# Kernel tuning notes

Hardware: AMD Instinct MI355X
Metric: run time of the kernel (lower is better)

Reference implementation:

```python
import jax, jax.numpy as jnp
import numpy as np

B, T, C = 2, 2048, 1024
H = 16
HD = C // H  # 64
SCALE = 0.1 / (HD ** 0.5)


def setup_inputs() -> dict:
    key = jax.random.key(0)
    k1, k2, k3 = jax.random.split(key, 3)
    x = jax.random.normal(k1, (B, T, C), dtype=jnp.float32)
    W_attn = jax.random.normal(k2, (C, 3 * C), dtype=jnp.float32) * (C ** -0.5)
    b_attn = jnp.zeros((3 * C,), dtype=jnp.float32)
    W_proj = jax.random.normal(k3, (C, C), dtype=jnp.float32) * (C ** -0.5)
    b_proj = jnp.zeros((C,), dtype=jnp.float32)
    return {"x": x, "W_attn": W_attn, "b_attn": b_attn, "W_proj": W_proj, "b_proj": b_proj}


def reference(x, W_attn, b_attn, W_proj, b_proj):
    Bx, Tx, Cx = x.shape
    qkv = x @ W_attn + b_attn  # [B,T,3C]
    q, k, v = jnp.split(qkv, 3, axis=-1)
    # [B,T,C] -> [B,H,T,HD]
    q = q.reshape(Bx, Tx, H, HD).transpose(0, 2, 1, 3)
    k = k.reshape(Bx, Tx, H, HD).transpose(0, 2, 1, 3)
    v = v.reshape(Bx, Tx, H, HD).transpose(0, 2, 1, 3)
    # note the extra 0.1 factor baked into this module's scaling
    attn = jnp.einsum('bhqd,bhkd->bhqk', q, k) * SCALE
    causal = jnp.tril(jnp.ones((Tx, Tx), dtype=bool))
    attn = jnp.where(causal[None, None, :, :], attn, -jnp.inf)
    attn = jax.nn.softmax(attn, axis=-1)
    y = jnp.einsum('bhqk,bhkd->bhqd', attn, v)
    y = y.transpose(0, 2, 1, 3).reshape(Bx, Tx, Cx)
    return y @ W_proj + b_proj
```

## Files before the change

### kernel.cpp

```cpp
#include <hip/hip_runtime.h>

typedef unsigned short u16;
typedef unsigned int u32;
typedef float f32x4 __attribute__((ext_vector_type(4)));
typedef float f32x16 __attribute__((ext_vector_type(16)));
typedef __bf16 bf16x8 __attribute__((ext_vector_type(8)));
typedef u16 u16x8 __attribute__((ext_vector_type(8)));
typedef u32 u32x4 __attribute__((ext_vector_type(4)));

#define ATT_SCALE 0.0125f
#define LOG2E 1.4426950408889634f

__device__ __forceinline__ u16 f2bf(float x) {
  unsigned u = __builtin_bit_cast(unsigned, x);
  u += 0x7fffu + ((u >> 16) & 1u);
  return (u16)(u >> 16);
}

__device__ __forceinline__ u32 pack_bf16(float lo, float hi) {
  __bf16 a = (__bf16)lo, b = (__bf16)hi;
  return ((u32)__builtin_bit_cast(u16, b) << 16) | __builtin_bit_cast(u16, a);
}

__device__ __forceinline__ float fexp2(float x) {
  return __builtin_amdgcn_exp2f(x);
}

__device__ __forceinline__ f32x4 mfma16(u16x8 a, u16x8 b, f32x4 c) {
  return __builtin_amdgcn_mfma_f32_16x16x32_bf16(
      __builtin_bit_cast(bf16x8, a), __builtin_bit_cast(bf16x8, b), c, 0, 0, 0);
}

__device__ __forceinline__ f32x16 mfma32(u16x8 a, u16x8 b, f32x16 c) {
  return __builtin_amdgcn_mfma_f32_32x32x16_bf16(
      __builtin_bit_cast(bf16x8, a), __builtin_bit_cast(bf16x8, b), c, 0, 0, 0);
}

__device__ __forceinline__ void gl_lds16(const void* g, void* l) {
  __builtin_amdgcn_global_load_lds(
      (__attribute__((address_space(1))) void*)g,
      (__attribute__((address_space(3))) void*)l, 16, 0, 0);
}

__global__ void k_pre(const float* __restrict__ x, const float* __restrict__ W_attn,
                      const float* __restrict__ W_proj, u16* __restrict__ x_bf,
                      u16* __restrict__ Wt_a, u16* __restrict__ Wt_p) {
  __shared__ float tile[32][33];
  const int id = blockIdx.x, tid = threadIdx.x;
  if (id < 2048) {
    int base = id * 2048 + tid * 4;
#pragma unroll
    for (int s = 0; s < 2; ++s) {
      int i = base + s * 1024;
      float4 v = *(const float4*)&x[i];
      ushort4 o;
      o.x = f2bf(v.x); o.y = f2bf(v.y); o.z = f2bf(v.z); o.w = f2bf(v.w);
      *(ushort4*)&x_bf[i] = o;
    }
    return;
  }
  const float* in;
  u16* outp;
  int rows, cols, bx, by;
  if (id < 5120) {
    int t2 = id - 2048;
    bx = t2 % 96; by = t2 / 96;
    in = W_attn; outp = Wt_a; rows = 1024; cols = 3072;
  } else {
    int t3 = id - 5120;
    bx = t3 & 31; by = t3 >> 5;
    in = W_proj; outp = Wt_p; rows = 1024; cols = 1024;
  }
  int tx = tid & 31, ty = tid >> 5;
  int n0 = bx * 32, k0 = by * 32;
#pragma unroll
  for (int i = 0; i < 32; i += 8)
    tile[ty + i][tx] = in[(size_t)(k0 + ty + i) * cols + n0 + tx];
  __syncthreads();
#pragma unroll
  for (int i = 0; i < 32; i += 8)
    outp[(size_t)(n0 + ty + i) * rows + k0 + tx] = f2bf(tile[tx][ty + i]);
}

__global__ void k_gemm_qkv(const u16* __restrict__ A, const u16* __restrict__ Bt,
                           const float* __restrict__ bias,
                           u16* __restrict__ qb, u16* __restrict__ kb, u16* __restrict__ vTb) {
  __shared__ u16 Al[128 * 64];
  __shared__ u16 Bl[128 * 64];
  const int tid = threadIdx.x;
  const int lane = tid & 63;
  const int w = tid >> 6;
  const int m0 = blockIdx.y * 128;
  const int n0 = blockIdx.x * 128;
  const int wr = (w >> 1) * 64;
  const int wc = (w & 1) * 64;
  const int lr = lane & 15;
  const int lk = (lane >> 4) * 8;

  f32x4 acc[4][4] = {};

  for (int k0 = 0; k0 < 1024; k0 += 64) {
#pragma unroll
    for (int it = 0; it < 4; ++it) {
      int off = (it * 256 + tid) * 8;
      int r = off >> 6, c = off & 63;
      gl_lds16(&A[(size_t)(m0 + r) * 1024 + k0 + c], &Al[off]);
      gl_lds16(&Bt[(size_t)(n0 + r) * 1024 + k0 + c], &Bl[off]);
    }
    __syncthreads();
#pragma unroll
    for (int kk = 0; kk < 64; kk += 32) {
      u16x8 af[4], bf[4];
#pragma unroll
      for (int i = 0; i < 4; ++i) {
        af[i] = *(const u16x8*)&Al[(wr + i * 16 + lr) * 64 + kk + lk];
        bf[i] = *(const u16x8*)&Bl[(wc + i * 16 + lr) * 64 + kk + lk];
      }
#pragma unroll
      for (int i = 0; i < 4; ++i)
#pragma unroll
        for (int j = 0; j < 4; ++j)
          acc[i][j] = mfma16(af[i], bf[j], acc[i][j]);
    }
    __syncthreads();
  }

#pragma unroll
  for (int i = 0; i < 4; ++i) {
    int rowb = m0 + wr + i * 16 + ((lane >> 4) << 2);
#pragma unroll
    for (int j = 0; j < 4; ++j) {
      int col = n0 + wc + j * 16 + lr;
      float bv = bias[col];
      int which = col >> 10;
      int c = col & 1023;
      int h = c >> 6, d = c & 63;
      int b_ = rowb >> 11, t0 = rowb & 2047;
      int bh = b_ * 16 + h;
      if (which == 2) {
        ushort4 st;
        st.x = f2bf(acc[i][j][0] + bv);
        st.y = f2bf(acc[i][j][1] + bv);
        st.z = f2bf(acc[i][j][2] + bv);
        st.w = f2bf(acc[i][j][3] + bv);
        *(ushort4*)&vTb[((size_t)bh * 64 + d) * 2048 + t0] = st;
      } else {
        u16* dst = (which == 0) ? qb : kb;
        float sc = (which == 0) ? (ATT_SCALE * LOG2E) : 1.0f;
#pragma unroll
        for (int r = 0; r < 4; ++r) {
          float fv = (acc[i][j][r] + bv) * sc;
          dst[((size_t)bh * 2048 + t0 + r) * 64 + d] = f2bf(fv);
        }
      }
    }
  }
}

__device__ __forceinline__ void stage_pair(const u16* __restrict__ kb_bh,
                                           const u16* __restrict__ vT_bh,
                                           u16* Kd, u16* Vd, int kv0, int tid) {
#pragma unroll
  for (int it = 0; it < 4; ++it) {
    int ch = it * 256 + tid;
    int r = ch >> 3, c = ch & 7;
    gl_lds16(&kb_bh[(size_t)(kv0 + r) * 64 + (c ^ (r & 7)) * 8], &Kd[ch * 8]);
    int r2 = ch >> 4, c2 = ch & 15;
    int h2 = c2 >> 3, cc = c2 & 7;
    gl_lds16(&vT_bh[(size_t)r2 * 2048 + kv0 + (h2 * 8 + (cc ^ (r2 & 7))) * 8],
             &Vd[ch * 8]);
  }
}

__global__ __launch_bounds__(256) void k_attn(const u16* __restrict__ qb,
                                              const u16* __restrict__ kb,
                                              const u16* __restrict__ vTb,
                                              u16* __restrict__ yb) {
  __shared__ u16 Kl[2][8192];
  __shared__ u16 Vl[2][8192];

  const int tid = threadIdx.x, lane = tid & 63, w = tid >> 6;
  const int wq = w & 1;
  const int wp = w >> 1;
  const int id = blockIdx.x;
  const int bh = (id & 7) + ((id >> 7) << 3);
  const int pairi = (id >> 3) & 15;
  const int b_ = bh >> 4, h = bh & 15;
  const int ql = lane & 31;
  const int hi = lane >> 5;

  const u16* kb_bh = kb + (size_t)bh * 2048 * 64;
  const u16* vT_bh = vTb + (size_t)bh * 64 * 2048;

#pragma unroll 1
  for (int phase = 0; phase < 2; ++phase) {
    const int qt = phase ? (31 - pairi) : pairi;
    const int q0w = qt * 64 + wq * 32;
    const int qg = q0w + ql;
    const int lim = wq * 32 + ql;

    const u16* qrow = qb + ((size_t)bh * 2048 + qg) * 64;
    u16x8 qf[4];
#pragma unroll
    for (int ks = 0; ks < 4; ++ks)
      qf[ks] = *(const u16x8*)&qrow[ks * 16 + hi * 8];

    f32x16 o0 = {}, o1 = {};
    float mrow = -1e30f, lrow = 0.f;

    const int nkv = qt + 1;
    const int niter = (nkv + 1) >> 1;
    stage_pair(kb_bh, vT_bh, Kl[0], Vl[0], 0, tid);
    __syncthreads();
    int cur = 0;

    for (int it = 0; it < niter; ++it) {
      if (it + 1 < niter)
        stage_pair(kb_bh, vT_bh, Kl[cur ^ 1], Vl[cur ^ 1], (it + 1) * 128, tid);

      const int mytile = 2 * it + wp;
      if (mytile <= qt) {
        const u16* Kc = Kl[cur];
        const u16* Vc = Vl[cur];
        const int rbase = wp * 64;

        f32x16 s0 = {}, s1 = {};
        __builtin_amdgcn_s_setprio(1);
#pragma unroll
        for (int ks = 0; ks < 4; ++ks) {
          int ch = 2 * ks + hi;
          int r0 = rbase + ql, r1 = rbase + 32 + ql;
          u16x8 kf0 = *(const u16x8*)&Kc[r0 * 64 + ((ch ^ (r0 & 7)) * 8)];
          u16x8 kf1 = *(const u16x8*)&Kc[r1 * 64 + ((ch ^ (r1 & 7)) * 8)];
          s0 = mfma32(kf0, qf[ks], s0);
          s1 = mfma32(kf1, qf[ks], s1);
        }
        __builtin_amdgcn_s_setprio(0);

        const bool diag = (mytile == qt);
        float pv[32];
        float tmax = -1e30f;
#pragma unroll
        for (int r = 0; r < 16; ++r) {
          float a = s0[r], b2 = s1[r];
          if (diag) {
            int kl0 = (r & 3) + 8 * (r >> 2) + 4 * hi;
            if (kl0 > lim) a = -1e30f;
            if (kl0 + 32 > lim) b2 = -1e30f;
          }
          pv[r] = a;
          pv[16 + r] = b2;
          tmax = fmaxf(tmax, fmaxf(a, b2));
        }
        float rmax = fmaxf(tmax, __shfl_xor(tmax, 32, 64));

        if (__any(rmax > mrow + 8.0f)) {
          float mn = fmaxf(mrow, rmax);
          float al = fexp2(mrow - mn);
          mrow = mn;
          lrow *= al;
#pragma unroll
          for (int r = 0; r < 16; ++r) { o0[r] *= al; o1[r] *= al; }
        }

        u32 pw[16];
#pragma unroll
        for (int j = 0; j < 16; ++j) {
          float e0 = fexp2(pv[2 * j] - mrow);
          float e1 = fexp2(pv[2 * j + 1] - mrow);
          lrow += e0 + e1;
          pw[j] = pack_bf16(e0, e1);
        }

#pragma unroll
        for (int tt = 0; tt < 2; ++tt)
#pragma unroll
          for (int u = 0; u < 2; ++u)
#pragma unroll
            for (int z = 0; z < 2; ++z) {
              int jA = tt * 8 + u * 4 + z;
              asm volatile("v_permlane32_swap_b32 %0, %1"
                           : "+v"(pw[jA]), "+v"(pw[jA + 2]));
            }

        __builtin_amdgcn_s_setprio(1);
#pragma unroll
        for (int ks = 0; ks < 4; ++ks) {
          u32x4 pwv = {pw[4 * ks], pw[4 * ks + 1], pw[4 * ks + 2], pw[4 * ks + 3]};
          u16x8 pfrag = __builtin_bit_cast(u16x8, pwv);
          int ch = 2 * ks + hi;
          int rv0 = ql, rv1 = 32 + ql;
          u16x8 vf0 = *(const u16x8*)&Vc[rv0 * 128 + (wp * 8 + (ch ^ (rv0 & 7))) * 8];
          u16x8 vf1 = *(const u16x8*)&Vc[rv1 * 128 + (wp * 8 + (ch ^ (rv1 & 7))) * 8];
          o0 = mfma32(vf0, pfrag, o0);
          o1 = mfma32(vf1, pfrag, o1);
        }
        __builtin_amdgcn_s_setprio(0);
      }
      __syncthreads();
      cur ^= 1;
    }

    float* mb = (float*)&Kl[0][0];
    if (wp == 1) {
      float4* dst = (float4*)&mb[(wq * 64 + lane) * 37];
      float4 hd; hd.x = mrow; hd.y = lrow; hd.z = 0.f; hd.w = 0.f;
      dst[0] = hd;
#pragma unroll
      for (int j = 0; j < 4; ++j) {
        float4 t0 = {o0[4 * j], o0[4 * j + 1], o0[4 * j + 2], o0[4 * j + 3]};
        float4 t1 = {o1[4 * j], o1[4 * j + 1], o1[4 * j + 2], o1[4 * j + 3]};
        dst[1 + j] = t0;
        dst[5 + j] = t1;
      }
    }
    __syncthreads();
    if (wp == 0) {
      const float4* src = (const float4*)&mb[(wq * 64 + lane) * 37];
      float4 hd = src[0];
      float m2 = hd.x, l2 = hd.y;
      float m = fmaxf(mrow, m2);
      float a1 = fexp2(mrow - m), a2 = fexp2(m2 - m);
      float l = lrow * a1 + l2 * a2;
      l += __shfl_xor(l, 32, 64);
      float inv = 1.0f / l;

      size_t ybase = ((size_t)b_ * 2048 + qg) * 1024 + h * 64;
#pragma unroll
      for (int dt = 0; dt < 2; ++dt) {
#pragma unroll
        for (int rg = 0; rg < 4; ++rg) {
          float4 po = src[1 + dt * 4 + rg];
          const f32x16& ov = dt ? o1 : o0;
          int d0 = dt * 32 + 8 * rg + 4 * hi;
          ushort4 st;
          st.x = f2bf((ov[rg * 4 + 0] * a1 + po.x * a2) * inv);
          st.y = f2bf((ov[rg * 4 + 1] * a1 + po.y * a2) * inv);
          st.z = f2bf((ov[rg * 4 + 2] * a1 + po.z * a2) * inv);
          st.w = f2bf((ov[rg * 4 + 3] * a1 + po.w * a2) * inv);
          *(ushort4*)&yb[ybase + d0] = st;
        }
      }
    }
    __syncthreads();
  }
}

__global__ void k_gemm_out(const u16* __restrict__ A, const u16* __restrict__ Bt,
                           const float* __restrict__ bias, float* __restrict__ out) {
  __shared__ u16 Al[64 * 64];
  __shared__ u16 Bl[128 * 64];
  const int tid = threadIdx.x;
  const int lane = tid & 63;
  const int w = tid >> 6;
  const int m0 = blockIdx.y * 64;
  const int n0 = blockIdx.x * 128;
  const int wr = (w >> 1) * 32;
  const int wc = (w & 1) * 64;
  const int lr = lane & 15;
  const int lk = (lane >> 4) * 8;

  f32x4 acc[2][4] = {};

  for (int k0 = 0; k0 < 1024; k0 += 64) {
#pragma unroll
    for (int it = 0; it < 2; ++it) {
      int ch = it * 256 + tid;
      int r = ch >> 3, c = (ch & 7) * 8;
      gl_lds16(&A[(size_t)(m0 + r) * 1024 + k0 + c], &Al[ch * 8]);
    }
#pragma unroll
    for (int it = 0; it < 4; ++it) {
      int ch = it * 256 + tid;
      int r = ch >> 3, c = (ch & 7) * 8;
      gl_lds16(&Bt[(size_t)(n0 + r) * 1024 + k0 + c], &Bl[ch * 8]);
    }
    __syncthreads();
#pragma unroll
    for (int kk = 0; kk < 64; kk += 32) {
      u16x8 af[2], bf[4];
#pragma unroll
      for (int i = 0; i < 2; ++i)
        af[i] = *(const u16x8*)&Al[(wr + i * 16 + lr) * 64 + kk + lk];
#pragma unroll
      for (int j = 0; j < 4; ++j)
        bf[j] = *(const u16x8*)&Bl[(wc + j * 16 + lr) * 64 + kk + lk];
#pragma unroll
      for (int i = 0; i < 2; ++i)
#pragma unroll
        for (int j = 0; j < 4; ++j)
          acc[i][j] = mfma16(af[i], bf[j], acc[i][j]);
    }
    __syncthreads();
  }

#pragma unroll
  for (int i = 0; i < 2; ++i) {
    int rowb = m0 + wr + i * 16 + ((lane >> 4) << 2);
#pragma unroll
    for (int j = 0; j < 4; ++j) {
      int col = n0 + wc + j * 16 + lr;
      float bv = bias[col];
#pragma unroll
      for (int r = 0; r < 4; ++r)
        out[(size_t)(rowb + r) * 1024 + col] = acc[i][j][r] + bv;
    }
  }
}

extern "C" void kernel_launch(void* const* d_in, const int* in_sizes, int n_in,
                              void* d_out, int out_size, void* d_ws, size_t ws_size,
                              hipStream_t stream) {
  const float* x      = (const float*)d_in[0];
  const float* W_attn = (const float*)d_in[1];
  const float* b_attn = (const float*)d_in[2];
  const float* W_proj = (const float*)d_in[3];
  const float* b_proj = (const float*)d_in[4];
  float* out = (float*)d_out;

  char* ws = (char*)d_ws;
  const size_t MB = 1024 * 1024;
  u16* x_bf  = (u16*)(ws);
  u16* Wt_a  = (u16*)(ws + 8 * MB);
  u16* Wt_p  = (u16*)(ws + 14 * MB);
  u16* qbf   = (u16*)(ws + 16 * MB);
  u16* kbf   = (u16*)(ws + 24 * MB);
  u16* vTbf  = (u16*)(ws + 32 * MB);
  u16* ybf   = (u16*)(ws + 40 * MB);

  k_pre<<<6144, 256, 0, stream>>>(x, W_attn, W_proj, x_bf, Wt_a, Wt_p);
  k_gemm_qkv<<<dim3(24, 32), 256, 0, stream>>>(x_bf, Wt_a, b_attn, qbf, kbf, vTbf);
  k_attn<<<512, 256, 0, stream>>>(qbf, kbf, vTbf, ybf);
  k_gemm_out<<<dim3(8, 64), 256, 0, stream>>>(ybf, Wt_p, b_proj, out);
}
```

Measured before the change: 112.4 us.

## Split attention KV tile across 8 waves with 4-way partial softmax merge

Doubles the attention block to 512 threads so each 64-key KV tile is split into two 32-key halves handled by separate waves, giving four independent softmax partials per query group. A three-step online-softmax merge through LDS then combines them. Each wave does half the QK and PV MFMA work per tile, which cuts per-wave latency and register pressure. In exchange it adds more merge traffic, more exp/rescale work and a larger block that may lower occupancy.

```diff
diff --git a/kernel.cpp b/kernel.cpp
--- a/kernel.cpp
+++ b/kernel.cpp
@@ -161,8 +161,8 @@
                                            const u16* __restrict__ vT_bh,
                                            u16* Kd, u16* Vd, int kv0, int tid) {
 #pragma unroll
-  for (int it = 0; it < 4; ++it) {
-    int ch = it * 256 + tid;
+  for (int it = 0; it < 2; ++it) {
+    int ch = it * 512 + tid;
     int r = ch >> 3, c = ch & 7;
     gl_lds16(&kb_bh[(size_t)(kv0 + r) * 64 + (c ^ (r & 7)) * 8], &Kd[ch * 8]);
     int r2 = ch >> 4, c2 = ch & 15;
@@ -172,16 +172,17 @@
   }
 }
 
-__global__ __launch_bounds__(256) void k_attn(const u16* __restrict__ qb,
+__global__ __launch_bounds__(512) void k_attn(const u16* __restrict__ qb,
                                               const u16* __restrict__ kb,
                                               const u16* __restrict__ vTb,
                                               u16* __restrict__ yb) {
-  __shared__ u16 Kl[2][8192];
-  __shared__ u16 Vl[2][8192];
+  __shared__ u16 lds_[32768];
 
   const int tid = threadIdx.x, lane = tid & 63, w = tid >> 6;
   const int wq = w & 1;
-  const int wp = w >> 1;
+  const int pid = w >> 1;
+  const int wp = pid & 1;
+  const int wk = pid >> 1;
   const int id = blockIdx.x;
   const int bh = (id & 7) + ((id >> 7) << 3);
   const int pairi = (id >> 3) & 15;
@@ -210,47 +211,42 @@
 
     const int nkv = qt + 1;
     const int niter = (nkv + 1) >> 1;
-    stage_pair(kb_bh, vT_bh, Kl[0], Vl[0], 0, tid);
+    stage_pair(kb_bh, vT_bh, lds_, lds_ + 16384, 0, tid);
     __syncthreads();
     int cur = 0;
 
     for (int it = 0; it < niter; ++it) {
       if (it + 1 < niter)
-        stage_pair(kb_bh, vT_bh, Kl[cur ^ 1], Vl[cur ^ 1], (it + 1) * 128, tid);
+        stage_pair(kb_bh, vT_bh, lds_ + (cur ^ 1) * 8192,
+                   lds_ + 16384 + (cur ^ 1) * 8192, (it + 1) * 128, tid);
 
       const int mytile = 2 * it + wp;
       if (mytile <= qt) {
-        const u16* Kc = Kl[cur];
-        const u16* Vc = Vl[cur];
-        const int rbase = wp * 64;
-
-        f32x16 s0 = {}, s1 = {};
+        const u16* Kc = lds_ + cur * 8192;
+        const u16* Vc = lds_ + 16384 + cur * 8192;
+        const int rk = wp * 64 + wk * 32 + ql;
+
+        f32x16 s0 = {};
         __builtin_amdgcn_s_setprio(1);
 #pragma unroll
         for (int ks = 0; ks < 4; ++ks) {
           int ch = 2 * ks + hi;
-          int r0 = rbase + ql, r1 = rbase + 32 + ql;
-          u16x8 kf0 = *(const u16x8*)&Kc[r0 * 64 + ((ch ^ (r0 & 7)) * 8)];
-          u16x8 kf1 = *(const u16x8*)&Kc[r1 * 64 + ((ch ^ (r1 & 7)) * 8)];
-          s0 = mfma32(kf0, qf[ks], s0);
-          s1 = mfma32(kf1, qf[ks], s1);
+          u16x8 kf = *(const u16x8*)&Kc[rk * 64 + ((ch ^ (rk & 7)) * 8)];
+          s0 = mfma32(kf, qf[ks], s0);
         }
         __builtin_amdgcn_s_setprio(0);
 
         const bool diag = (mytile == qt);
-        float pv[32];
         float tmax = -1e30f;
 #pragma unroll
         for (int r = 0; r < 16; ++r) {
-          float a = s0[r], b2 = s1[r];
+          float a = s0[r];
           if (diag) {
-            int kl0 = (r & 3) + 8 * (r >> 2) + 4 * hi;
-            if (kl0 > lim) a = -1e30f;
-            if (kl0 + 32 > lim) b2 = -1e30f;
+            int kl = wk * 32 + (r & 3) + 8 * (r >> 2) + 4 * hi;
+            if (kl > lim) a = -1e30f;
+            s0[r] = a;
           }
-          pv[r] = a;
-          pv[16 + r] = b2;
-          tmax = fmaxf(tmax, fmaxf(a, b2));
+          tmax = fmaxf(tmax, a);
         }
         float rmax = fmaxf(tmax, __shfl_xor(tmax, 32, 64));
 
@@ -263,35 +259,31 @@
           for (int r = 0; r < 16; ++r) { o0[r] *= al; o1[r] *= al; }
         }
 
-        u32 pw[16];
-#pragma unroll
-        for (int j = 0; j < 16; ++j) {
-          float e0 = fexp2(pv[2 * j] - mrow);
-          float e1 = fexp2(pv[2 * j + 1] - mrow);
+        u32 pw[8];
+#pragma unroll
+        for (int j = 0; j < 8; ++j) {
+          float e0 = fexp2(s0[2 * j] - mrow);
+          float e1 = fexp2(s0[2 * j + 1] - mrow);
           lrow += e0 + e1;
           pw[j] = pack_bf16(e0, e1);
         }
 
 #pragma unroll
-        for (int tt = 0; tt < 2; ++tt)
-#pragma unroll
-          for (int u = 0; u < 2; ++u)
-#pragma unroll
-            for (int z = 0; z < 2; ++z) {
-              int jA = tt * 8 + u * 4 + z;
-              asm volatile("v_permlane32_swap_b32 %0, %1"
-                           : "+v"(pw[jA]), "+v"(pw[jA + 2]));
-            }
+        for (int g = 0; g < 2; ++g)
+#pragma unroll
+          for (int z = 0; z < 2; ++z)
+            asm volatile("v_permlane32_swap_b32 %0, %1"
+                         : "+v"(pw[g * 4 + z]), "+v"(pw[g * 4 + z + 2]));
 
         __builtin_amdgcn_s_setprio(1);
 #pragma unroll
-        for (int ks = 0; ks < 4; ++ks) {
+        for (int ks = 0; ks < 2; ++ks) {
           u32x4 pwv = {pw[4 * ks], pw[4 * ks + 1], pw[4 * ks + 2], pw[4 * ks + 3]};
           u16x8 pfrag = __builtin_bit_cast(u16x8, pwv);
-          int ch = 2 * ks + hi;
+          int cc = wk * 4 + 2 * ks + hi;
           int rv0 = ql, rv1 = 32 + ql;
-          u16x8 vf0 = *(const u16x8*)&Vc[rv0 * 128 + (wp * 8 + (ch ^ (rv0 & 7))) * 8];
-          u16x8 vf1 = *(const u16x8*)&Vc[rv1 * 128 + (wp * 8 + (ch ^ (rv1 & 7))) * 8];
+          u16x8 vf0 = *(const u16x8*)&Vc[rv0 * 128 + (wp * 8 + (cc ^ (rv0 & 7))) * 8];
+          u16x8 vf1 = *(const u16x8*)&Vc[rv1 * 128 + (wp * 8 + (cc ^ (rv1 & 7))) * 8];
           o0 = mfma32(vf0, pfrag, o0);
           o1 = mfma32(vf1, pfrag, o1);
         }
@@ -301,9 +293,9 @@
       cur ^= 1;
     }
 
-    float* mb = (float*)&Kl[0][0];
-    if (wp == 1) {
-      float4* dst = (float4*)&mb[(wq * 64 + lane) * 37];
+    float* mb = (float*)lds_;
+    if (pid > 0) {
+      float4* dst = (float4*)&mb[((pid - 1) * 128 + wq * 64 + lane) * 37];
       float4 hd; hd.x = mrow; hd.y = lrow; hd.z = 0.f; hd.w = 0.f;
       dst[0] = hd;
 #pragma unroll
@@ -315,29 +307,45 @@
       }
     }
     __syncthreads();
-    if (wp == 0) {
-      const float4* src = (const float4*)&mb[(wq * 64 + lane) * 37];
-      float4 hd = src[0];
-      float m2 = hd.x, l2 = hd.y;
-      float m = fmaxf(mrow, m2);
-      float a1 = fexp2(mrow - m), a2 = fexp2(m2 - m);
-      float l = lrow * a1 + l2 * a2;
+    if (pid == 0) {
+      float m = mrow, l = lrow;
+#pragma unroll
+      for (int j = 0; j < 3; ++j) {
+        const float4* src = (const float4*)&mb[(j * 128 + wq * 64 + lane) * 37];
+        float4 hd = src[0];
+        float mn = fmaxf(m, hd.x);
+        float a = fexp2(m - mn), aj = fexp2(hd.x - mn);
+        l = l * a + hd.y * aj;
+        m = mn;
+#pragma unroll
+        for (int rg = 0; rg < 4; ++rg) {
+          float4 t0 = src[1 + rg];
+          float4 t1 = src[5 + rg];
+          o0[4 * rg + 0] = o0[4 * rg + 0] * a + t0.x * aj;
+          o0[4 * rg + 1] = o0[4 * rg + 1] * a + t0.y * aj;
+          o0[4 * rg + 2] = o0[4 * rg + 2] * a + t0.z * aj;
+          o0[4 * rg + 3] = o0[4 * rg + 3] * a + t0.w * aj;
+          o1[4 * rg + 0] = o1[4 * rg + 0] * a + t1.x * aj;
+          o1[4 * rg + 1] = o1[4 * rg + 1] * a + t1.y * aj;
+          o1[4 * rg + 2] = o1[4 * rg + 2] * a + t1.z * aj;
+          o1[4 * rg + 3] = o1[4 * rg + 3] * a + t1.w * aj;
+        }
+      }
       l += __shfl_xor(l, 32, 64);
       float inv = 1.0f / l;
 
       size_t ybase = ((size_t)b_ * 2048 + qg) * 1024 + h * 64;
 #pragma unroll
       for (int dt = 0; dt < 2; ++dt) {
+        const f32x16& ov = dt ? o1 : o0;
 #pragma unroll
         for (int rg = 0; rg < 4; ++rg) {
-          float4 po = src[1 + dt * 4 + rg];
-          const f32x16& ov = dt ? o1 : o0;
           int d0 = dt * 32 + 8 * rg + 4 * hi;
           ushort4 st;
-          st.x = f2bf((ov[rg * 4 + 0] * a1 + po.x * a2) * inv);
-          st.y = f2bf((ov[rg * 4 + 1] * a1 + po.y * a2) * inv);
-          st.z = f2bf((ov[rg * 4 + 2] * a1 + po.z * a2) * inv);
-          st.w = f2bf((ov[rg * 4 + 3] * a1 + po.w * a2) * inv);
+          st.x = f2bf(ov[rg * 4 + 0] * inv);
+          st.y = f2bf(ov[rg * 4 + 1] * inv);
+          st.z = f2bf(ov[rg * 4 + 2] * inv);
+          st.w = f2bf(ov[rg * 4 + 3] * inv);
           *(ushort4*)&yb[ybase + d0] = st;
         }
       }
@@ -430,6 +438,6 @@
 
   k_pre<<<6144, 256, 0, stream>>>(x, W_attn, W_proj, x_bf, Wt_a, Wt_p);
   k_gemm_qkv<<<dim3(24, 32), 256, 0, stream>>>(x_bf, Wt_a, b_attn, qbf, kbf, vTbf);
-  k_attn<<<512, 256, 0, stream>>>(qbf, kbf, vTbf, ybf);
+  k_attn<<<512, 512, 0, stream>>>(qbf, kbf, vTbf, ybf);
   k_gemm_out<<<dim3(8, 64), 256, 0, stream>>>(ybf, Wt_p, b_proj, out);
 }
```

Measured after the change: 124.9 us. 1.11x slower.

## Split attention into 32-row query blocks, stage only K in LDS, read V directly

Applied to the files above, without the earlier changes.

The attention kernel drops the paired-tile, two-phase 256-thread blocks and launches 2048 blocks of 128 threads. Each block handles one 32-row query tile, with its two waves splitting the KV tiles and merging their partials at the end. Only K is staged through LDS. V fragments are now loaded straight from global memory into registers before the softmax, which halves LDS use and should raise occupancy. The risks are that K tiles are loaded redundantly by more blocks, V reads become uncoalesced global loads, and load balance now relies on heavy-first block ordering rather than pairing.

```diff
diff --git a/kernel.cpp b/kernel.cpp
--- a/kernel.cpp
+++ b/kernel.cpp
@@ -157,34 +157,27 @@
   }
 }
 
-__device__ __forceinline__ void stage_pair(const u16* __restrict__ kb_bh,
-                                           const u16* __restrict__ vT_bh,
-                                           u16* Kd, u16* Vd, int kv0, int tid) {
-#pragma unroll
-  for (int it = 0; it < 4; ++it) {
-    int ch = it * 256 + tid;
+__device__ __forceinline__ void stage_k(const u16* __restrict__ kb_bh,
+                                        u16* Kd, int kv0, int tid) {
+#pragma unroll
+  for (int it = 0; it < 8; ++it) {
+    int ch = it * 128 + tid;
     int r = ch >> 3, c = ch & 7;
     gl_lds16(&kb_bh[(size_t)(kv0 + r) * 64 + (c ^ (r & 7)) * 8], &Kd[ch * 8]);
-    int r2 = ch >> 4, c2 = ch & 15;
-    int h2 = c2 >> 3, cc = c2 & 7;
-    gl_lds16(&vT_bh[(size_t)r2 * 2048 + kv0 + (h2 * 8 + (cc ^ (r2 & 7))) * 8],
-             &Vd[ch * 8]);
-  }
-}
-
-__global__ __launch_bounds__(256) void k_attn(const u16* __restrict__ qb,
+  }
+}
+
+__global__ __launch_bounds__(128) void k_attn(const u16* __restrict__ qb,
                                               const u16* __restrict__ kb,
                                               const u16* __restrict__ vTb,
                                               u16* __restrict__ yb) {
   __shared__ u16 Kl[2][8192];
-  __shared__ u16 Vl[2][8192];
-
-  const int tid = threadIdx.x, lane = tid & 63, w = tid >> 6;
-  const int wq = w & 1;
-  const int wp = w >> 1;
+
+  const int tid = threadIdx.x, lane = tid & 63;
+  const int wp = tid >> 6;
   const int id = blockIdx.x;
-  const int bh = (id & 7) + ((id >> 7) << 3);
-  const int pairi = (id >> 3) & 15;
+  const int bh = id & 31;
+  const int qt = 63 - (id >> 5);
   const int b_ = bh >> 4, h = bh & 15;
   const int ql = lane & 31;
   const int hi = lane >> 5;
@@ -192,157 +185,162 @@
   const u16* kb_bh = kb + (size_t)bh * 2048 * 64;
   const u16* vT_bh = vTb + (size_t)bh * 64 * 2048;
 
-#pragma unroll 1
-  for (int phase = 0; phase < 2; ++phase) {
-    const int qt = phase ? (31 - pairi) : pairi;
-    const int q0w = qt * 64 + wq * 32;
-    const int qg = q0w + ql;
-    const int lim = wq * 32 + ql;
-
-    const u16* qrow = qb + ((size_t)bh * 2048 + qg) * 64;
-    u16x8 qf[4];
-#pragma unroll
-    for (int ks = 0; ks < 4; ++ks)
-      qf[ks] = *(const u16x8*)&qrow[ks * 16 + hi * 8];
-
-    f32x16 o0 = {}, o1 = {};
-    float mrow = -1e30f, lrow = 0.f;
-
-    const int nkv = qt + 1;
-    const int niter = (nkv + 1) >> 1;
-    stage_pair(kb_bh, vT_bh, Kl[0], Vl[0], 0, tid);
+  const int q0 = qt * 32;
+  const int qg = q0 + ql;
+  const int lim = (qt & 1) * 32 + ql;
+  const int nkv = (qt >> 1) + 1;
+  const int niter = (nkv + 1) >> 1;
+
+  const u16* qrow = qb + ((size_t)bh * 2048 + qg) * 64;
+  u16x8 qf[4];
+#pragma unroll
+  for (int ks = 0; ks < 4; ++ks)
+    qf[ks] = *(const u16x8*)&qrow[ks * 16 + hi * 8];
+
+  f32x16 o0 = {}, o1 = {};
+  float mrow = -1e30f, lrow = 0.f;
+
+  stage_k(kb_bh, Kl[0], 0, tid);
+  __syncthreads();
+  int cur = 0;
+
+  for (int it = 0; it < niter; ++it) {
+    if (it + 1 < niter)
+      stage_k(kb_bh, Kl[cur ^ 1], (it + 1) * 128, tid);
+
+    const int mytile = 2 * it + wp;
+    if (mytile < nkv) {
+      const u16* Kc = Kl[cur];
+      const int kv0 = mytile * 64;
+      const int rk0 = wp * 64 + ql, rk1 = wp * 64 + 32 + ql;
+
+      f32x16 s0 = {}, s1 = {};
+      __builtin_amdgcn_s_setprio(1);
+#pragma unroll
+      for (int ks = 0; ks < 4; ++ks) {
+        int ch = 2 * ks + hi;
+        u16x8 kf0 = *(const u16x8*)&Kc[rk0 * 64 + ((ch ^ (rk0 & 7)) * 8)];
+        u16x8 kf1 = *(const u16x8*)&Kc[rk1 * 64 + ((ch ^ (rk1 & 7)) * 8)];
+        s0 = mfma32(kf0, qf[ks], s0);
+        s1 = mfma32(kf1, qf[ks], s1);
+      }
+      __builtin_amdgcn_s_setprio(0);
+
+      const u16* vr0 = vT_bh + (size_t)ql * 2048 + kv0;
+      const u16* vr1 = vr0 + (size_t)32 * 2048;
+      u16x8 vf0[4], vf1[4];
+#pragma unroll
+      for (int ks = 0; ks < 4; ++ks) {
+        vf0[ks] = *(const u16x8*)(vr0 + ks * 16 + hi * 8);
+        vf1[ks] = *(const u16x8*)(vr1 + ks * 16 + hi * 8);
+      }
+
+      const bool diag = (mytile == nkv - 1);
+      float tmax = -1e30f;
+#pragma unroll
+      for (int r = 0; r < 16; ++r) {
+        float a = s0[r], b2 = s1[r];
+        if (diag) {
+          int kl0 = (r & 3) + 8 * (r >> 2) + 4 * hi;
+          if (kl0 > lim) a = -1e30f;
+          if (kl0 + 32 > lim) b2 = -1e30f;
+          s0[r] = a;
+          s1[r] = b2;
+        }
+        tmax = fmaxf(tmax, fmaxf(a, b2));
+      }
+      float rmax = fmaxf(tmax, __shfl_xor(tmax, 32, 64));
+
+      if (__any(rmax > mrow + 8.0f)) {
+        float mn = fmaxf(mrow, rmax);
+        float al = fexp2(mrow - mn);
+        mrow = mn;
+        lrow *= al;
+#pragma unroll
+        for (int r = 0; r < 16; ++r) { o0[r] *= al; o1[r] *= al; }
+      }
+
+      u32 pw[16];
+#pragma unroll
+      for (int j = 0; j < 8; ++j) {
+        float e0 = fexp2(s0[2 * j] - mrow);
+        float e1 = fexp2(s0[2 * j + 1] - mrow);
+        lrow += e0 + e1;
+        pw[j] = pack_bf16(e0, e1);
+      }
+#pragma unroll
+      for (int j = 0; j < 8; ++j) {
+        float e0 = fexp2(s1[2 * j] - mrow);
+        float e1 = fexp2(s1[2 * j + 1] - mrow);
+        lrow += e0 + e1;
+        pw[8 + j] = pack_bf16(e0, e1);
+      }
+
+#pragma unroll
+      for (int tt = 0; tt < 2; ++tt)
+#pragma unroll
+        for (int u = 0; u < 2; ++u)
+#pragma unroll
+          for (int z = 0; z < 2; ++z) {
+            int jA = tt * 8 + u * 4 + z;
+            asm volatile("v_permlane32_swap_b32 %0, %1"
+                         : "+v"(pw[jA]), "+v"(pw[jA + 2]));
+          }
+
+      __builtin_amdgcn_s_setprio(1);
+#pragma unroll
+      for (int ks = 0; ks < 4; ++ks) {
+        u32x4 pwv = {pw[4 * ks], pw[4 * ks + 1], pw[4 * ks + 2], pw[4 * ks + 3]};
+        u16x8 pfrag = __builtin_bit_cast(u16x8, pwv);
+        o0 = mfma32(vf0[ks], pfrag, o0);
+        o1 = mfma32(vf1[ks], pfrag, o1);
+      }
+      __builtin_amdgcn_s_setprio(0);
+    }
     __syncthreads();
-    int cur = 0;
-
-    for (int it = 0; it < niter; ++it) {
-      if (it + 1 < niter)
-        stage_pair(kb_bh, vT_bh, Kl[cur ^ 1], Vl[cur ^ 1], (it + 1) * 128, tid);
-
-      const int mytile = 2 * it + wp;
-      if (mytile <= qt) {
-        const u16* Kc = Kl[cur];
-        const u16* Vc = Vl[cur];
-        const int rbase = wp * 64;
-
-        f32x16 s0 = {}, s1 = {};
-        __builtin_amdgcn_s_setprio(1);
-#pragma unroll
-        for (int ks = 0; ks < 4; ++ks) {
-          int ch = 2 * ks + hi;
-          int r0 = rbase + ql, r1 = rbase + 32 + ql;
-          u16x8 kf0 = *(const u16x8*)&Kc[r0 * 64 + ((ch ^ (r0 & 7)) * 8)];
-          u16x8 kf1 = *(const u16x8*)&Kc[r1 * 64 + ((ch ^ (r1 & 7)) * 8)];
-          s0 = mfma32(kf0, qf[ks], s0);
-          s1 = mfma32(kf1, qf[ks], s1);
-        }
-        __builtin_amdgcn_s_setprio(0);
-
-        const bool diag = (mytile == qt);
-        float pv[32];
-        float tmax = -1e30f;
-#pragma unroll
-        for (int r = 0; r < 16; ++r) {
-          float a = s0[r], b2 = s1[r];
-          if (diag) {
-            int kl0 = (r & 3) + 8 * (r >> 2) + 4 * hi;
-            if (kl0 > lim) a = -1e30f;
-            if (kl0 + 32 > lim) b2 = -1e30f;
-          }
-          pv[r] = a;
-          pv[16 + r] = b2;
-          tmax = fmaxf(tmax, fmaxf(a, b2));
-        }
-        float rmax = fmaxf(tmax, __shfl_xor(tmax, 32, 64));
-
-        if (__any(rmax > mrow + 8.0f)) {
-          float mn = fmaxf(mrow, rmax);
-          float al = fexp2(mrow - mn);
-          mrow = mn;
-          lrow *= al;
-#pragma unroll
-          for (int r = 0; r < 16; ++r) { o0[r] *= al; o1[r] *= al; }
-        }
-
-        u32 pw[16];
-#pragma unroll
-        for (int j = 0; j < 16; ++j) {
-          float e0 = fexp2(pv[2 * j] - mrow);
-          float e1 = fexp2(pv[2 * j + 1] - mrow);
-          lrow += e0 + e1;
-          pw[j] = pack_bf16(e0, e1);
-        }
-
-#pragma unroll
-        for (int tt = 0; tt < 2; ++tt)
-#pragma unroll
-          for (int u = 0; u < 2; ++u)
-#pragma unroll
-            for (int z = 0; z < 2; ++z) {
-              int jA = tt * 8 + u * 4 + z;
-              asm volatile("v_permlane32_swap_b32 %0, %1"
-                           : "+v"(pw[jA]), "+v"(pw[jA + 2]));
-            }
-
-        __builtin_amdgcn_s_setprio(1);
-#pragma unroll
-        for (int ks = 0; ks < 4; ++ks) {
-          u32x4 pwv = {pw[4 * ks], pw[4 * ks + 1], pw[4 * ks + 2], pw[4 * ks + 3]};
-          u16x8 pfrag = __builtin_bit_cast(u16x8, pwv);
-          int ch = 2 * ks + hi;
-          int rv0 = ql, rv1 = 32 + ql;
-          u16x8 vf0 = *(const u16x8*)&Vc[rv0 * 128 + (wp * 8 + (ch ^ (rv0 & 7))) * 8];
-          u16x8 vf1 = *(const u16x8*)&Vc[rv1 * 128 + (wp * 8 + (ch ^ (rv1 & 7))) * 8];
-          o0 = mfma32(vf0, pfrag, o0);
-          o1 = mfma32(vf1, pfrag, o1);
-        }
-        __builtin_amdgcn_s_setprio(0);
-      }
-      __syncthreads();
-      cur ^= 1;
-    }
-
-    float* mb = (float*)&Kl[0][0];
-    if (wp == 1) {
-      float4* dst = (float4*)&mb[(wq * 64 + lane) * 37];
-      float4 hd; hd.x = mrow; hd.y = lrow; hd.z = 0.f; hd.w = 0.f;
-      dst[0] = hd;
-#pragma unroll
-      for (int j = 0; j < 4; ++j) {
-        float4 t0 = {o0[4 * j], o0[4 * j + 1], o0[4 * j + 2], o0[4 * j + 3]};
-        float4 t1 = {o1[4 * j], o1[4 * j + 1], o1[4 * j + 2], o1[4 * j + 3]};
-        dst[1 + j] = t0;
-        dst[5 + j] = t1;
-      }
-    }
-    __syncthreads();
-    if (wp == 0) {
-      const float4* src = (const float4*)&mb[(wq * 64 + lane) * 37];
-      float4 hd = src[0];
-      float m2 = hd.x, l2 = hd.y;
-      float m = fmaxf(mrow, m2);
-      float a1 = fexp2(mrow - m), a2 = fexp2(m2 - m);
-      float l = lrow * a1 + l2 * a2;
-      l += __shfl_xor(l, 32, 64);
-      float inv = 1.0f / l;
-
-      size_t ybase = ((size_t)b_ * 2048 + qg) * 1024 + h * 64;
-#pragma unroll
-      for (int dt = 0; dt < 2; ++dt) {
-#pragma unroll
-        for (int rg = 0; rg < 4; ++rg) {
-          float4 po = src[1 + dt * 4 + rg];
-          const f32x16& ov = dt ? o1 : o0;
-          int d0 = dt * 32 + 8 * rg + 4 * hi;
-          ushort4 st;
-          st.x = f2bf((ov[rg * 4 + 0] * a1 + po.x * a2) * inv);
-          st.y = f2bf((ov[rg * 4 + 1] * a1 + po.y * a2) * inv);
-          st.z = f2bf((ov[rg * 4 + 2] * a1 + po.z * a2) * inv);
-          st.w = f2bf((ov[rg * 4 + 3] * a1 + po.w * a2) * inv);
-          *(ushort4*)&yb[ybase + d0] = st;
-        }
-      }
-    }
-    __syncthreads();
+    cur ^= 1;
+  }
+
+  float* mb = (float*)&Kl[0][0];
+  if (wp == 1) {
+    float4* dst = (float4*)&mb[lane * 37];
+    float4 hd; hd.x = mrow; hd.y = lrow; hd.z = 0.f; hd.w = 0.f;
+    dst[0] = hd;
+#pragma unroll
+    for (int j = 0; j < 4; ++j) {
+      float4 t0 = {o0[4 * j], o0[4 * j + 1], o0[4 * j + 2], o0[4 * j + 3]};
+      float4 t1 = {o1[4 * j], o1[4 * j + 1], o1[4 * j + 2], o1[4 * j + 3]};
+      dst[1 + j] = t0;
+      dst[5 + j] = t1;
+    }
+  }
+  __syncthreads();
+  if (wp == 0) {
+    const float4* src = (const float4*)&mb[lane * 37];
+    float4 hd = src[0];
+    float m2 = hd.x, l2 = hd.y;
+    float m = fmaxf(mrow, m2);
+    float a1 = fexp2(mrow - m), a2 = fexp2(m2 - m);
+    float l = lrow * a1 + l2 * a2;
+    l += __shfl_xor(l, 32, 64);
+    float inv = 1.0f / l;
+
+    size_t ybase = ((size_t)b_ * 2048 + qg) * 1024 + h * 64;
+#pragma unroll
+    for (int dt = 0; dt < 2; ++dt) {
+      const f32x16& ov = dt ? o1 : o0;
+#pragma unroll
+      for (int rg = 0; rg < 4; ++rg) {
+        float4 po = src[1 + dt * 4 + rg];
+        int d0 = dt * 32 + 8 * rg + 4 * hi;
+        ushort4 st;
+        st.x = f2bf((ov[rg * 4 + 0] * a1 + po.x * a2) * inv);
+        st.y = f2bf((ov[rg * 4 + 1] * a1 + po.y * a2) * inv);
+        st.z = f2bf((ov[rg * 4 + 2] * a1 + po.z * a2) * inv);
+        st.w = f2bf((ov[rg * 4 + 3] * a1 + po.w * a2) * inv);
+        *(ushort4*)&yb[ybase + d0] = st;
+      }
+    }
   }
 }
 
@@ -430,6 +428,6 @@
 
   k_pre<<<6144, 256, 0, stream>>>(x, W_attn, W_proj, x_bf, Wt_a, Wt_p);
   k_gemm_qkv<<<dim3(24, 32), 256, 0, stream>>>(x_bf, Wt_a, b_attn, qbf, kbf, vTbf);
-  k_attn<<<512, 256, 0, stream>>>(qbf, kbf, vTbf, ybf);
+  k_attn<<<2048, 128, 0, stream>>>(qbf, kbf, vTbf, ybf);
   k_gemm_out<<<dim3(8, 64), 256, 0, stream>>>(ybf, Wt_p, b_proj, out);
 }
```

Measured after the change: 166.9 us. 1.48x slower.

## Split KV range across four wave pairs and drop double-buffering in attention

Applied to the files above, without the earlier changes.

The attention block grows from 256 to 512 threads so four wave pairs each take a different 64-row KV tile per iteration, loading 256 KV rows at once into one LDS buffer. The previous double-buffered prefetch is replaced by a load-sync-compute-sync loop, and the final merge combines three partial softmax states instead of one. The aim is more parallelism per block for the long causal rows. The cost is exposed global-load latency with no prefetch, and more idle waves on the diagonal and short-row tiles.

```diff
diff --git a/kernel.cpp b/kernel.cpp
--- a/kernel.cpp
+++ b/kernel.cpp
@@ -157,27 +157,26 @@
   }
 }
 
-__device__ __forceinline__ void stage_pair(const u16* __restrict__ kb_bh,
+__device__ __forceinline__ void stage_quad(const u16* __restrict__ kb_bh,
                                            const u16* __restrict__ vT_bh,
                                            u16* Kd, u16* Vd, int kv0, int tid) {
 #pragma unroll
   for (int it = 0; it < 4; ++it) {
-    int ch = it * 256 + tid;
+    int ch = it * 512 + tid;
     int r = ch >> 3, c = ch & 7;
     gl_lds16(&kb_bh[(size_t)(kv0 + r) * 64 + (c ^ (r & 7)) * 8], &Kd[ch * 8]);
-    int r2 = ch >> 4, c2 = ch & 15;
-    int h2 = c2 >> 3, cc = c2 & 7;
-    gl_lds16(&vT_bh[(size_t)r2 * 2048 + kv0 + (h2 * 8 + (cc ^ (r2 & 7))) * 8],
+    int r2 = ch >> 5, c2 = ch & 31;
+    int qtr = c2 >> 3, cc = c2 & 7;
+    gl_lds16(&vT_bh[(size_t)r2 * 2048 + kv0 + qtr * 64 + (cc ^ (r2 & 7)) * 8],
              &Vd[ch * 8]);
   }
 }
 
-__global__ __launch_bounds__(256) void k_attn(const u16* __restrict__ qb,
+__global__ __launch_bounds__(512) void k_attn(const u16* __restrict__ qb,
                                               const u16* __restrict__ kb,
                                               const u16* __restrict__ vTb,
                                               u16* __restrict__ yb) {
-  __shared__ u16 Kl[2][8192];
-  __shared__ u16 Vl[2][8192];
+  __shared__ u16 lds_[32768];
 
   const int tid = threadIdx.x, lane = tid & 63, w = tid >> 6;
   const int wq = w & 1;
@@ -209,19 +208,17 @@
     float mrow = -1e30f, lrow = 0.f;
 
     const int nkv = qt + 1;
-    const int niter = (nkv + 1) >> 1;
-    stage_pair(kb_bh, vT_bh, Kl[0], Vl[0], 0, tid);
-    __syncthreads();
-    int cur = 0;
-
+    const int niter = (nkv + 3) >> 2;
+
+#pragma unroll 1
     for (int it = 0; it < niter; ++it) {
-      if (it + 1 < niter)
-        stage_pair(kb_bh, vT_bh, Kl[cur ^ 1], Vl[cur ^ 1], (it + 1) * 128, tid);
-
-      const int mytile = 2 * it + wp;
+      stage_quad(kb_bh, vT_bh, lds_, lds_ + 16384, it * 256, tid);
+      __syncthreads();
+
+      const int mytile = 4 * it + wp;
       if (mytile <= qt) {
-        const u16* Kc = Kl[cur];
-        const u16* Vc = Vl[cur];
+        const u16* Kc = lds_;
+        const u16* Vc = lds_ + 16384;
         const int rbase = wp * 64;
 
         f32x16 s0 = {}, s1 = {};
@@ -290,20 +287,19 @@
           u16x8 pfrag = __builtin_bit_cast(u16x8, pwv);
           int ch = 2 * ks + hi;
           int rv0 = ql, rv1 = 32 + ql;
-          u16x8 vf0 = *(const u16x8*)&Vc[rv0 * 128 + (wp * 8 + (ch ^ (rv0 & 7))) * 8];
-          u16x8 vf1 = *(const u16x8*)&Vc[rv1 * 128 + (wp * 8 + (ch ^ (rv1 & 7))) * 8];
+          u16x8 vf0 = *(const u16x8*)&Vc[rv0 * 256 + (wp * 8 + (ch ^ (rv0 & 7))) * 8];
+          u16x8 vf1 = *(const u16x8*)&Vc[rv1 * 256 + (wp * 8 + (ch ^ (rv1 & 7))) * 8];
           o0 = mfma32(vf0, pfrag, o0);
           o1 = mfma32(vf1, pfrag, o1);
         }
         __builtin_amdgcn_s_setprio(0);
       }
       __syncthreads();
-      cur ^= 1;
-    }
-
-    float* mb = (float*)&Kl[0][0];
-    if (wp == 1) {
-      float4* dst = (float4*)&mb[(wq * 64 + lane) * 37];
+    }
+
+    float* mb = (float*)lds_;
+    if (wp > 0) {
+      float4* dst = (float4*)&mb[((wp - 1) * 128 + wq * 64 + lane) * 37];
       float4 hd; hd.x = mrow; hd.y = lrow; hd.z = 0.f; hd.w = 0.f;
       dst[0] = hd;
 #pragma unroll
@@ -316,28 +312,44 @@
     }
     __syncthreads();
     if (wp == 0) {
-      const float4* src = (const float4*)&mb[(wq * 64 + lane) * 37];
-      float4 hd = src[0];
-      float m2 = hd.x, l2 = hd.y;
-      float m = fmaxf(mrow, m2);
-      float a1 = fexp2(mrow - m), a2 = fexp2(m2 - m);
-      float l = lrow * a1 + l2 * a2;
+      float m = mrow, l = lrow;
+#pragma unroll
+      for (int j = 0; j < 3; ++j) {
+        const float4* src = (const float4*)&mb[(j * 128 + wq * 64 + lane) * 37];
+        float4 hd = src[0];
+        float mn = fmaxf(m, hd.x);
+        float a = fexp2(m - mn), aj = fexp2(hd.x - mn);
+        l = l * a + hd.y * aj;
+        m = mn;
+#pragma unroll
+        for (int rg = 0; rg < 4; ++rg) {
+          float4 t0 = src[1 + rg];
+          float4 t1 = src[5 + rg];
+          o0[4 * rg + 0] = o0[4 * rg + 0] * a + t0.x * aj;
+          o0[4 * rg + 1] = o0[4 * rg + 1] * a + t0.y * aj;
+          o0[4 * rg + 2] = o0[4 * rg + 2] * a + t0.z * aj;
+          o0[4 * rg + 3] = o0[4 * rg + 3] * a + t0.w * aj;
+          o1[4 * rg + 0] = o1[4 * rg + 0] * a + t1.x * aj;
+          o1[4 * rg + 1] = o1[4 * rg + 1] * a + t1.y * aj;
+          o1[4 * rg + 2] = o1[4 * rg + 2] * a + t1.z * aj;
+          o1[4 * rg + 3] = o1[4 * rg + 3] * a + t1.w * aj;
+        }
+      }
       l += __shfl_xor(l, 32, 64);
       float inv = 1.0f / l;
 
       size_t ybase = ((size_t)b_ * 2048 + qg) * 1024 + h * 64;
 #pragma unroll
       for (int dt = 0; dt < 2; ++dt) {
+        const f32x16& ov = dt ? o1 : o0;
 #pragma unroll
         for (int rg = 0; rg < 4; ++rg) {
-          float4 po = src[1 + dt * 4 + rg];
-          const f32x16& ov = dt ? o1 : o0;
           int d0 = dt * 32 + 8 * rg + 4 * hi;
           ushort4 st;
-          st.x = f2bf((ov[rg * 4 + 0] * a1 + po.x * a2) * inv);
-          st.y = f2bf((ov[rg * 4 + 1] * a1 + po.y * a2) * inv);
-          st.z = f2bf((ov[rg * 4 + 2] * a1 + po.z * a2) * inv);
-          st.w = f2bf((ov[rg * 4 + 3] * a1 + po.w * a2) * inv);
+          st.x = f2bf(ov[rg * 4 + 0] * inv);
+          st.y = f2bf(ov[rg * 4 + 1] * inv);
+          st.z = f2bf(ov[rg * 4 + 2] * inv);
+          st.w = f2bf(ov[rg * 4 + 3] * inv);
           *(ushort4*)&yb[ybase + d0] = st;
         }
       }
@@ -430,6 +442,6 @@
 
   k_pre<<<6144, 256, 0, stream>>>(x, W_attn, W_proj, x_bf, Wt_a, Wt_p);
   k_gemm_qkv<<<dim3(24, 32), 256, 0, stream>>>(x_bf, Wt_a, b_attn, qbf, kbf, vTbf);
-  k_attn<<<512, 256, 0, stream>>>(qbf, kbf, vTbf, ybf);
+  k_attn<<<512, 512, 0, stream>>>(qbf, kbf, vTbf, ybf);
   k_gemm_out<<<dim3(8, 64), 256, 0, stream>>>(ybf, Wt_p, b_proj, out);
 }
```

Measured after the change: 125.1 us. +11.2%, slower.
